# Kernel optimization log

Measured on AMD Instinct MI355X. Metric: run time of the kernel, lower is better.

Reference implementation:

```python
import jax, jax.numpy as jnp
import numpy as np

B, S, D = 16, 2048, 1024
E2 = 2 * 2048  # embed_dim * 2 FFN hidden
EPS = 1e-5


def layernorm(x, g, b):
    mu = jnp.mean(x, axis=-1, keepdims=True)
    var = jnp.mean(jnp.square(x - mu), axis=-1, keepdims=True)
    return (x - mu) * jax.lax.rsqrt(var + EPS) * g + b


def setup_inputs() -> dict:
    key = jax.random.key(0)
    ks = jax.random.split(key, 4)
    lags = jax.random.normal(ks[0], (B, S, D), dtype=jnp.float32)
    W1 = jax.random.normal(ks[1], (D, E2), dtype=jnp.float32) * (1.0 / np.sqrt(D))
    b1 = jnp.zeros((E2,), dtype=jnp.float32)
    W2 = jax.random.normal(ks[2], (E2, D), dtype=jnp.float32) * (1.0 / np.sqrt(E2))
    b2 = jnp.zeros((D,), dtype=jnp.float32)
    g1 = jnp.ones((D,), dtype=jnp.float32)
    be1 = jnp.zeros((D,), dtype=jnp.float32)
    g3 = jnp.ones((D,), dtype=jnp.float32)
    be3 = jnp.zeros((D,), dtype=jnp.float32)
    return {"lags": lags, "W1": W1, "b1": b1, "W2": W2, "b2": b2,
            "g1": g1, "be1": be1, "g3": g3, "be3": be3}


def reference(lags, W1, b1, W2, b2, g1, be1, g3, be3):
    # manual self-attention: scores = lags @ lags^T / sqrt(D)  -> [B,S,S]
    scale = 1.0 / jnp.sqrt(jnp.asarray(D, dtype=lags.dtype))
    scores = jnp.einsum('bsd,btd->bst', lags, lags) * scale
    attn = jax.nn.softmax(scores, axis=-1)
    attn_out = jnp.einsum('bst,btd->bsd', attn, lags)  # [B,S,D]
    x = layernorm(lags + attn_out, g1, be1)
    # FFN: Linear -> exact GELU -> Linear (dropout=0)
    h = jax.nn.gelu(jnp.einsum('bsd,de->bse', x, W1) + b1, approximate=False)
    ff = jnp.einsum('bse,ed->bsd', h, W2) + b2
    return layernorm(x + ff, g3, be3)
```

## Files before the change

kernel.cpp:

```cpp
#include <hip/hip_runtime.h>
#include <hip/hip_bf16.h>
#include <cmath>


typedef __bf16 bf16;
typedef __attribute__((ext_vector_type(8))) __bf16 bf16x8;
typedef __attribute__((ext_vector_type(4))) __bf16 bf16x4;
typedef __attribute__((ext_vector_type(4))) float f32x4;

static constexpr int kB  = 16;
static constexpr int kS  = 2048;
static constexpr int kD  = 1024;
static constexpr int kE2 = 4096;
static constexpr int kCB = 8;
static constexpr int kFR = 16384;

__device__ __forceinline__ void gload_lds16(const bf16* g, bf16* l) {
    __builtin_amdgcn_global_load_lds(
        (const __attribute__((address_space(1))) void*)g,
        (__attribute__((address_space(3))) void*)l,
        16, 0, 0);
}

__global__ __launch_bounds__(256) void cvt_bf16_kernel(const float* __restrict__ in,
                                                       bf16* __restrict__ out) {
    size_t i = ((size_t)blockIdx.x * 256 + threadIdx.x) * 4;
    float4 v = *(const float4*)(in + i);
    bf16x4 o;
    o.x = (bf16)v.x; o.y = (bf16)v.y; o.z = (bf16)v.z; o.w = (bf16)v.w;
    *(bf16x4*)(out + i) = o;
}

__global__ void transpose_cvt_kernel(const float* __restrict__ in, bf16* __restrict__ out,
                                     int R, int C, long long sIn, long long sOut) {
    __shared__ float tile[32][33];
    in  += (size_t)blockIdx.z * sIn;
    out += (size_t)blockIdx.z * sOut;
    const int c0 = blockIdx.x * 32, r0 = blockIdx.y * 32;
    const int tx = threadIdx.x, ty = threadIdx.y;
#pragma unroll
    for (int k = 0; k < 32; k += 8)
        tile[ty + k][tx] = in[(size_t)(r0 + ty + k) * C + (c0 + tx)];
    __syncthreads();
#pragma unroll
    for (int k = 0; k < 32; k += 8)
        out[(size_t)(c0 + ty + k) * R + (r0 + tx)] = (bf16)tile[tx][ty + k];
}

template <int MODE>
__global__ __launch_bounds__(512, 2)
void gemm_bt_kernel(const bf16* __restrict__ A, const bf16* __restrict__ Bm,
                    float* __restrict__ C, bf16* __restrict__ Cb,
                    const float* __restrict__ bias,
                    const float* __restrict__ resF, const bf16* __restrict__ resB,
                    int N, int K,
                    long long sA, long long sB, long long sC, long long sRes,
                    float scale) {
    __shared__ __align__(16) bf16 lds[2][2][2][256 * 32];
    const int tid  = threadIdx.x;
    const int lane = tid & 63;
    const int wv   = tid >> 6;
    const int wm   = wv >> 2;
    const int wn   = wv & 3;
    const int quad = lane >> 4, l15 = lane & 15;
    const long long z = blockIdx.z;
    const bf16* Ab = A  + z * sA + (size_t)blockIdx.y * 256 * K;
    const bf16* Bb = Bm + z * sB + (size_t)blockIdx.x * 256 * K;

    const bf16* gA = Ab + (size_t)(wv * 32 + (lane >> 2)) * K + (lane & 3) * 8;
    const bf16* gB = Bb + (size_t)(wv * 32 + (lane >> 2)) * K + (lane & 3) * 8;
    const int NT = K >> 6;

    f32x4 acc[8][4];
#pragma unroll
    for (int i = 0; i < 8; i++)
#pragma unroll
        for (int j = 0; j < 4; j++) {
            f32x4 zv = {0.0f, 0.0f, 0.0f, 0.0f};
            acc[i][j] = zv;
        }

#define STAGE_HALF(h_)                                                        \
    do {                                                                      \
        const int t_ = (h_) >> 2, sel_ = (h_) & 3;                            \
        const bf16* g_ = ((sel_ & 1) ? gB : gA) + t_ * 64 + (sel_ >> 1) * 32; \
        bf16* l_ = &lds[t_ & 1][sel_ & 1][sel_ >> 1][wv * 32 * 32];           \
        gload_lds16(g_, l_);                                                  \
        gload_lds16(g_ + (size_t)16 * K, l_ + 16 * 32);                       \
    } while (0)

#define GPHASE(BUF, KS, QM, READB)                                            \
    do {                                                                      \
        if (READB) {                                                          \
            _Pragma("unroll")                                                 \
            for (int nf = 0; nf < 4; nf++)                                    \
                bfr[nf] = *(const bf16x8*)&lds[BUF][1][KS][                   \
                    (wn * 64 + nf * 16 + l15) * 32 + quad * 8];               \
        }                                                                     \
        _Pragma("unroll")                                                     \
        for (int mf = 0; mf < 4; mf++)                                        \
            afr[mf] = *(const bf16x8*)&lds[BUF][0][KS][                       \
                (wm * 128 + (QM * 4 + mf) * 16 + l15) * 32 + quad * 8];       \
        if (h < 4 * NT) STAGE_HALF(h);                                        \
        h++;                                                                  \
        asm volatile("" ::: "memory");                                        \
        __builtin_amdgcn_s_barrier();                                         \
        asm volatile("" ::: "memory");                                        \
        __builtin_amdgcn_s_setprio(1);                                        \
        _Pragma("unroll")                                                     \
        for (int mf = 0; mf < 4; mf++)                                        \
            _Pragma("unroll")                                                 \
            for (int nf = 0; nf < 4; nf++)                                    \
                acc[QM * 4 + mf][nf] = __builtin_amdgcn_mfma_f32_16x16x32_bf16( \
                    afr[mf], bfr[nf], acc[QM * 4 + mf][nf], 0, 0, 0);         \
        __builtin_amdgcn_s_setprio(0);                                        \
        asm volatile("s_waitcnt vmcnt(6)" ::: "memory");                      \
        __builtin_amdgcn_s_barrier();                                         \
        asm volatile("" ::: "memory");                                        \
    } while (0)

    bf16x8 afr[4], bfr[4];
    int h = 0;
#pragma unroll
    for (int p = 0; p < 6; p++) { STAGE_HALF(h); h++; }
    asm volatile("s_waitcnt vmcnt(4)" ::: "memory");
    __builtin_amdgcn_s_barrier();
    asm volatile("" ::: "memory");

    for (int i = 0; i < NT / 2; i++) {
        GPHASE(0, 0, 0, true);
        GPHASE(0, 0, 1, false);
        GPHASE(0, 1, 0, true);
        GPHASE(0, 1, 1, false);
        GPHASE(1, 0, 0, true);
        GPHASE(1, 0, 1, false);
        GPHASE(1, 1, 0, true);
        GPHASE(1, 1, 1, false);
    }
#undef GPHASE
#undef STAGE_HALF

    const size_t m0 = (size_t)blockIdx.y * 256 + wm * 128;
    const size_t n0 = (size_t)blockIdx.x * 256 + wn * 64;
#pragma unroll
    for (int nf = 0; nf < 4; nf++) {
        const size_t col = n0 + nf * 16 + l15;
        const float bcol = (MODE == 2 || MODE == 3) ? bias[col] : 0.0f;
#pragma unroll
        for (int mf = 0; mf < 8; mf++) {
#pragma unroll
            for (int rr = 0; rr < 4; rr++) {
                const size_t row = m0 + mf * 16 + quad * 4 + rr;
                const float v = acc[mf][nf][rr];
                if (MODE == 0) {
                    Cb[z * sC + row * N + col] = (bf16)(v * scale);
                } else if (MODE == 1) {
                    C[z * sC + row * N + col] = v + resF[z * sRes + row * N + col];
                } else if (MODE == 2) {
                    const float t = v + bcol;
                    const float gl = 0.5f * t * (1.0f + erff(t * 0.70710678118654752f));
                    Cb[row * N + col] = (bf16)gl;
                } else {
                    C[row * N + col] = v + bcol + (float)resB[row * N + col];
                }
            }
        }
    }
}

__global__ __launch_bounds__(256)
void softmax_bf16_kernel(bf16* __restrict__ SP) {
    __shared__ float red[8];
    const size_t row = blockIdx.x;
    bf16* p = SP + row * kS;
    const int tid = threadIdx.x;
    bf16x8 v = *(const bf16x8*)(p + tid * 8);
    float f[8];
#pragma unroll
    for (int i = 0; i < 8; i++) f[i] = (float)v[i];
    float m = f[0];
#pragma unroll
    for (int i = 1; i < 8; i++) m = fmaxf(m, f[i]);
#pragma unroll
    for (int o = 32; o > 0; o >>= 1) m = fmaxf(m, __shfl_down(m, o, 64));
    if ((tid & 63) == 0) red[tid >> 6] = m;
    __syncthreads();
    m = fmaxf(fmaxf(red[0], red[1]), fmaxf(red[2], red[3]));
    float e[8], s = 0.0f;
#pragma unroll
    for (int i = 0; i < 8; i++) { e[i] = __expf(f[i] - m); s += e[i]; }
#pragma unroll
    for (int o = 32; o > 0; o >>= 1) s += __shfl_down(s, o, 64);
    __syncthreads();
    if ((tid & 63) == 0) red[4 + (tid >> 6)] = s;
    __syncthreads();
    s = red[4] + red[5] + red[6] + red[7];
    const float inv = 1.0f / s;
    bf16x8 o;
#pragma unroll
    for (int i = 0; i < 8; i++) o[i] = (bf16)(e[i] * inv);
    *(bf16x8*)(p + tid * 8) = o;
}

__global__ __launch_bounds__(256)
void layernorm_kernel(const float* __restrict__ in, const float* __restrict__ g,
                      const float* __restrict__ be, float* __restrict__ outF,
                      bf16* __restrict__ outB) {
    __shared__ float red[8];
    const size_t row = blockIdx.x;
    const float* src = in + row * kD;
    const int tid = threadIdx.x;
    float4 v = *(const float4*)(src + tid * 4);
    float s = v.x + v.y + v.z + v.w;
#pragma unroll
    for (int o = 32; o > 0; o >>= 1) s += __shfl_down(s, o, 64);
    if ((tid & 63) == 0) red[tid >> 6] = s;
    __syncthreads();
    const float mu = (red[0] + red[1] + red[2] + red[3]) * (1.0f / kD);
    const float d0 = v.x - mu, d1 = v.y - mu, d2 = v.z - mu, d3 = v.w - mu;
    float ss = d0 * d0 + d1 * d1 + d2 * d2 + d3 * d3;
#pragma unroll
    for (int o = 32; o > 0; o >>= 1) ss += __shfl_down(ss, o, 64);
    __syncthreads();
    if ((tid & 63) == 0) red[4 + (tid >> 6)] = ss;
    __syncthreads();
    const float var = (red[4] + red[5] + red[6] + red[7]) * (1.0f / kD);
    const float rstd = rsqrtf(var + 1e-5f);
    float4 gg = *(const float4*)(g + tid * 4);
    float4 bb = *(const float4*)(be + tid * 4);
    float4 o;
    o.x = d0 * rstd * gg.x + bb.x;
    o.y = d1 * rstd * gg.y + bb.y;
    o.z = d2 * rstd * gg.z + bb.z;
    o.w = d3 * rstd * gg.w + bb.w;
    if (outF) *(float4*)(outF + row * kD + tid * 4) = o;
    if (outB) {
        bf16x4 ob;
        ob.x = (bf16)o.x; ob.y = (bf16)o.y; ob.z = (bf16)o.z; ob.w = (bf16)o.w;
        *(bf16x4*)(outB + row * kD + tid * 4) = ob;
    }
}

extern "C" void kernel_launch(void* const* d_in, const int* in_sizes, int n_in,
                              void* d_out, int out_size, void* d_ws, size_t ws_size,
                              hipStream_t stream) {
    const float* lags = (const float*)d_in[0];
    const float* W1   = (const float*)d_in[1];
    const float* b1   = (const float*)d_in[2];
    const float* W2   = (const float*)d_in[3];
    const float* b2   = (const float*)d_in[4];
    const float* g1   = (const float*)d_in[5];
    const float* be1  = (const float*)d_in[6];
    const float* g3   = (const float*)d_in[7];
    const float* be3  = (const float*)d_in[8];
    float* out = (float*)d_out;

    const size_t REQUIRED = (size_t)(64 + 8 + 8 + 64 + 64) * 1024 * 1024;
    if (ws_size < REQUIRED) return;

    char* w = (char*)d_ws;
    bf16* lagsb = (bf16*)w; w += (size_t)kB * kS * kD * 2;
    bf16* W1T   = (bf16*)w; w += (size_t)kD * kE2 * 2;
    bf16* W2T   = (bf16*)w; w += (size_t)kE2 * kD * 2;
    bf16* lagsT = (bf16*)w; w += (size_t)kB * kD * kS * 2;
    bf16* SP    = (bf16*)w;
    bf16* xb    = lagsb;
    bf16* h     = lagsT;

    const int n = kB * kS * kD;

    cvt_bf16_kernel<<<n / 1024, 256, 0, stream>>>(lags, lagsb);
    transpose_cvt_kernel<<<dim3(kD / 32, kS / 32, kB), dim3(32, 8), 0, stream>>>(
        lags, lagsT, kS, kD, (long long)kS * kD, (long long)kD * kS);
    transpose_cvt_kernel<<<dim3(kE2 / 32, kD / 32, 1), dim3(32, 8), 0, stream>>>(
        W1, W1T, kD, kE2, 0, 0);
    transpose_cvt_kernel<<<dim3(kD / 32, kE2 / 32, 1), dim3(32, 8), 0, stream>>>(
        W2, W2T, kE2, kD, 0, 0);

    for (int c = 0; c < kB / kCB; c++) {
        const size_t off = (size_t)c * kCB * kS * kD;
        gemm_bt_kernel<0><<<dim3(kS / 256, kS / 256, kCB), 512, 0, stream>>>(
            lagsb + off, lagsb + off, nullptr, SP, nullptr, nullptr, nullptr,
            kS, kD, (long long)kS * kD, (long long)kS * kD, (long long)kS * kS, 0, 0.03125f);
        softmax_bf16_kernel<<<kCB * kS, 256, 0, stream>>>(SP);
        gemm_bt_kernel<1><<<dim3(kD / 256, kS / 256, kCB), 512, 0, stream>>>(
            SP, lagsT + off, out + off, nullptr, nullptr, lags + off, nullptr,
            kD, kS, (long long)kS * kS, (long long)kD * kS,
            (long long)kS * kD, (long long)kS * kD, 1.0f);
        layernorm_kernel<<<kCB * kS, 256, 0, stream>>>(out + off, g1, be1, nullptr, xb + off);
    }

    for (int c = 0; c < (kB * kS) / kFR; c++) {
        const size_t roff = (size_t)c * kFR * kD;
        gemm_bt_kernel<2><<<dim3(kE2 / 256, kFR / 256, 1), 512, 0, stream>>>(
            xb + roff, W1T, nullptr, h, b1, nullptr, nullptr,
            kE2, kD, 0, 0, 0, 0, 1.0f);
        gemm_bt_kernel<3><<<dim3(kD / 256, kFR / 256, 1), 512, 0, stream>>>(
            h, W2T, out + roff, nullptr, b2, nullptr, xb + roff,
            kD, kE2, 0, 0, 0, 0, 1.0f);
    }

    layernorm_kernel<<<kB * kS, 256, 0, stream>>>(out, g3, be3, out, nullptr);
}
```

Baseline: 1.676 ms.

## Swizzle GEMM LDS tiles and relax vmcnt waits to every other phase

Applies an XOR swizzle to the 16-byte column chunk when staging A/B tiles into LDS and when reading fragments, to spread ds_read accesses across banks and reduce bank conflicts. Adds an explicit lgkmcnt(0) wait plus a sched_barrier before the MFMA block so LDS reads finish before compute. Only issues the vmcnt(6) wait on every second phase, loosening the synchronisation on global-to-LDS loads. The relaxed vmcnt wait risks reading LDS data that has not arrived yet if the staging depth assumption is wrong.

```diff
diff --git a/kernel.cpp b/kernel.cpp
--- a/kernel.cpp
+++ b/kernel.cpp
@@ -63,12 +63,15 @@
     const int wm   = wv >> 2;
     const int wn   = wv & 3;
     const int quad = lane >> 4, l15 = lane & 15;
+    const int quadS = quad ^ ((l15 >> 1) & 3);
     const long long z = blockIdx.z;
     const bf16* Ab = A  + z * sA + (size_t)blockIdx.y * 256 * K;
     const bf16* Bb = Bm + z * sB + (size_t)blockIdx.x * 256 * K;
 
-    const bf16* gA = Ab + (size_t)(wv * 32 + (lane >> 2)) * K + (lane & 3) * 8;
-    const bf16* gB = Bb + (size_t)(wv * 32 + (lane >> 2)) * K + (lane & 3) * 8;
+    const int srow = wv * 32 + (lane >> 2);
+    const int scol = ((lane & 3) ^ ((lane >> 3) & 3)) * 8;
+    const bf16* gA = Ab + (size_t)srow * K + scol;
+    const bf16* gB = Bb + (size_t)srow * K + scol;
     const int NT = K >> 6;
 
     f32x4 acc[8][4];
@@ -89,23 +92,24 @@
         gload_lds16(g_ + (size_t)16 * K, l_ + 16 * 32);                       \
     } while (0)
 
-#define GPHASE(BUF, KS, QM, READB)                                            \
+#define GPHASE(BUF, KS, QM, READB, VM)                                        \
     do {                                                                      \
         if (READB) {                                                          \
             _Pragma("unroll")                                                 \
             for (int nf = 0; nf < 4; nf++)                                    \
                 bfr[nf] = *(const bf16x8*)&lds[BUF][1][KS][                   \
-                    (wn * 64 + nf * 16 + l15) * 32 + quad * 8];               \
+                    (wn * 64 + nf * 16 + l15) * 32 + quadS * 8];              \
         }                                                                     \
         _Pragma("unroll")                                                     \
         for (int mf = 0; mf < 4; mf++)                                        \
             afr[mf] = *(const bf16x8*)&lds[BUF][0][KS][                       \
-                (wm * 128 + (QM * 4 + mf) * 16 + l15) * 32 + quad * 8];       \
+                (wm * 128 + (QM * 4 + mf) * 16 + l15) * 32 + quadS * 8];      \
         if (h < 4 * NT) STAGE_HALF(h);                                        \
         h++;                                                                  \
         asm volatile("" ::: "memory");                                        \
         __builtin_amdgcn_s_barrier();                                         \
-        asm volatile("" ::: "memory");                                        \
+        asm volatile("s_waitcnt lgkmcnt(0)" ::: "memory");                    \
+        __builtin_amdgcn_sched_barrier(0);                                    \
         __builtin_amdgcn_s_setprio(1);                                        \
         _Pragma("unroll")                                                     \
         for (int mf = 0; mf < 4; mf++)                                        \
@@ -114,7 +118,7 @@
                 acc[QM * 4 + mf][nf] = __builtin_amdgcn_mfma_f32_16x16x32_bf16( \
                     afr[mf], bfr[nf], acc[QM * 4 + mf][nf], 0, 0, 0);         \
         __builtin_amdgcn_s_setprio(0);                                        \
-        asm volatile("s_waitcnt vmcnt(6)" ::: "memory");                      \
+        if (VM) asm volatile("s_waitcnt vmcnt(6)" ::: "memory");              \
         __builtin_amdgcn_s_barrier();                                         \
         asm volatile("" ::: "memory");                                        \
     } while (0)
@@ -128,14 +132,14 @@
     asm volatile("" ::: "memory");
 
     for (int i = 0; i < NT / 2; i++) {
-        GPHASE(0, 0, 0, true);
-        GPHASE(0, 0, 1, false);
-        GPHASE(0, 1, 0, true);
-        GPHASE(0, 1, 1, false);
-        GPHASE(1, 0, 0, true);
-        GPHASE(1, 0, 1, false);
-        GPHASE(1, 1, 0, true);
-        GPHASE(1, 1, 1, false);
+        GPHASE(0, 0, 0, true,  false);
+        GPHASE(0, 0, 1, false, true);
+        GPHASE(0, 1, 0, true,  false);
+        GPHASE(0, 1, 1, false, true);
+        GPHASE(1, 0, 0, true,  false);
+        GPHASE(1, 0, 1, false, true);
+        GPHASE(1, 1, 0, true,  false);
+        GPHASE(1, 1, 1, false, true);
     }
 #undef GPHASE
 #undef STAGE_HALF
```

Result: faster. 1.524 ms (-9.1%).
